# Optimization experiments

Hardware: AMD Instinct MI355X
Metric: run time of the kernel (lower is better)

## Reference

```python
import jax, jax.numpy as jnp
import numpy as np

TEMPERATURE = 0.5
EPS = 1e-8  # F.cosine_similarity default eps
NEG_FILL = -1e9  # fill_diagonal_(-1000000000.0)


def setup_inputs() -> dict:
    key = jax.random.key(0)
    k1, k2 = jax.random.split(key)
    N, D = 4096, 256
    zi = jax.random.normal(k1, (N, D), dtype=jnp.float32)
    zj = jax.random.normal(k2, (N, D), dtype=jnp.float32)
    return {"zi": zi, "zj": zj}


def reference(zi, zj):
    N = zi.shape[0]
    z = jnp.concatenate([zi, zj], axis=0)  # [2N, D]
    # cosine similarity: normalize once, then a single GEMM
    norms = jnp.sqrt(jnp.sum(z * z, axis=1, keepdims=True))
    zn = z / jnp.maximum(norms, EPS)
    sim = jnp.matmul(zn, zn.T) / TEMPERATURE  # [2N, 2N]
    idx = jnp.arange(2 * N)
    sim = sim.at[idx, idx].set(NEG_FILL)  # mask self-similarity
    labels = jnp.concatenate([jnp.arange(N) + N, jnp.arange(N)])
    # CrossEntropyLoss(reduction='sum'): sum_i (logsumexp(row_i) - row_i[label_i])
    logp = jax.nn.log_softmax(sim, axis=1)
    loss = -jnp.sum(logp[idx, labels])
    return loss / (2 * N)
```

## Files before the change

kernel.cpp:

```cpp
#include <hip/hip_runtime.h>
#include <hip/hip_bf16.h>
#include <math.h>


using short8  = __attribute__((ext_vector_type(8))) short;
using floatx4 = __attribute__((ext_vector_type(4))) float;

constexpr int TWO_N = 8192;
constexpr int DIM   = 256;
constexpr int NB    = 64;
constexpr int NTRI  = NB * (NB + 1) / 2;
constexpr float INV2N = 1.0f / 8192.0f;

__device__ static inline unsigned short f2bf(float f) {
  unsigned u = __float_as_uint(f);
  return (unsigned short)((u + 0x7fffu + ((u >> 16) & 1u)) >> 16);
}

__device__ static inline void async_copy16(const __hip_bfloat16* g, __hip_bfloat16* l) {
  __builtin_amdgcn_global_load_lds(
      (const __attribute__((address_space(1))) void*)(const void*)g,
      (__attribute__((address_space(3))) void*)(void*)l, 16, 0, 0);
}

__global__ __launch_bounds__(256) void k_normalize(
    const float* __restrict__ zi, const float* __restrict__ zj,
    __hip_bfloat16* __restrict__ zn, float* __restrict__ rowtotal,
    float* __restrict__ out)
{
  if (blockIdx.x == 0 && threadIdx.x == 0) out[0] = 0.0f;
  if (blockIdx.x < 32) rowtotal[blockIdx.x * 256 + threadIdx.x] = 0.0f;

  const int lane = threadIdx.x & 63;
  const int wave = threadIdx.x >> 6;
  const int row  = blockIdx.x * 4 + wave;
  const float* src = (row < 4096) ? (zi + (size_t)row * DIM)
                                  : (zj + (size_t)(row - 4096) * DIM);
  float4 v = reinterpret_cast<const float4*>(src)[lane];
  float ss = v.x * v.x + v.y * v.y + v.z * v.z + v.w * v.w;
#pragma unroll
  for (int m = 32; m >= 1; m >>= 1) ss += __shfl_xor(ss, m, 64);
  float inv = 1.0f / fmaxf(sqrtf(ss), 1e-8f);
  ushort4 o;
  o.x = f2bf(v.x * inv); o.y = f2bf(v.y * inv);
  o.z = f2bf(v.z * inv); o.w = f2bf(v.w * inv);
  reinterpret_cast<ushort4*>(zn + (size_t)row * DIM)[lane] = o;
}

__global__ __launch_bounds__(256) void k_simexp(
    const __hip_bfloat16* __restrict__ Z, float* __restrict__ rowtotal,
    float* __restrict__ out)
{
  __shared__ __align__(16) __hip_bfloat16 As[128 * 64];
  __shared__ __align__(16) __hip_bfloat16 Bs[128 * 64];
  __shared__ float rowsum[128];
  __shared__ float colsum[128];

  const int tid  = threadIdx.x;
  const int lane = tid & 63;
  const int wave = tid >> 6;
  const int wm   = wave >> 1;
  const int wn   = wave & 1;

  const int u = blockIdx.x;
  int jb = (int)((sqrtf(8.0f * (float)u + 1.0f) - 1.0f) * 0.5f);
  while ((jb + 1) * (jb + 2) / 2 <= u) ++jb;
  while (jb * (jb + 1) / 2 > u) --jb;
  const int ib = u - jb * (jb + 1) / 2;

  const bool diagblk = (ib == jb);
  const bool pairblk = (jb == ib + 32);
  const int i0 = ib * 128;
  const int j0 = jb * 128;

  if (tid < 128) { rowsum[tid] = 0.0f; colsum[tid] = 0.0f; }

  floatx4 acc[4][4] = {};

  const int lane7 = lane & 7;
  const int sub   = lane >> 3;
  const int gkoff = ((lane7 ^ sub) << 3);
  const int q     = lane >> 4;
  const int c16   = lane & 15;

  const __hip_bfloat16* gbase =
      Z + (size_t)((wave < 2 ? i0 : j0) + (wave & 1) * 64) * DIM;
  __hip_bfloat16* lbase = ((wave < 2) ? As : Bs) + (wave & 1) * 64 * 64;

  for (int kk = 0; kk < 4; ++kk) {
    const int k0 = kk * 64;
#pragma unroll
    for (int c = 0; c < 8; ++c) {
      const __hip_bfloat16* gp = gbase + (size_t)(c * 8 + sub) * DIM + k0 + gkoff;
      async_copy16(gp, lbase + c * 512);
    }
    __syncthreads();

#pragma unroll
    for (int ks = 0; ks < 2; ++ks) {
      const int phys = (ks * 4 + q) ^ lane7;
      short8 a[4], b[4];
#pragma unroll
      for (int mt = 0; mt < 4; ++mt)
        a[mt] = *reinterpret_cast<const short8*>(
            As + (wm * 64 + mt * 16 + c16) * 64 + phys * 8);
#pragma unroll
      for (int nt = 0; nt < 4; ++nt)
        b[nt] = *reinterpret_cast<const short8*>(
            Bs + (wn * 64 + nt * 16 + c16) * 64 + phys * 8);
#pragma unroll
      for (int mt = 0; mt < 4; ++mt)
#pragma unroll
        for (int nt = 0; nt < 4; ++nt)
          acc[mt][nt] = __builtin_amdgcn_mfma_f32_16x16x32_bf16(
              a[mt], b[nt], acc[mt][nt], 0, 0, 0);
    }
    __syncthreads();
  }

  float colacc[4] = {0.f, 0.f, 0.f, 0.f};
  float pc = 0.f;
  const bool diagwave = (wm == wn);

#pragma unroll
  for (int mt = 0; mt < 4; ++mt) {
#pragma unroll
    for (int reg = 0; reg < 4; ++reg) {
      const bool onquad = (c16 == q * 4 + reg);
      float s = 0.0f;
#pragma unroll
      for (int nt = 0; nt < 4; ++nt) {
        float e = __expf(2.0f * acc[mt][nt][reg] - 2.0f);
        bool skip = diagblk && diagwave && (nt == mt) && onquad;
        s += skip ? 0.0f : e;
        colacc[nt] += e;
      }
      if (pairblk && diagwave && onquad) pc += acc[mt][mt][reg];
      s += __shfl_xor(s, 1, 64);
      s += __shfl_xor(s, 2, 64);
      s += __shfl_xor(s, 4, 64);
      s += __shfl_xor(s, 8, 64);
      if (c16 == 0)
        atomicAdd(&rowsum[wm * 64 + mt * 16 + q * 4 + reg], s);
    }
  }

  if (!diagblk) {
#pragma unroll
    for (int nt = 0; nt < 4; ++nt) {
      float cs = colacc[nt];
      cs += __shfl_xor(cs, 16, 64);
      cs += __shfl_xor(cs, 32, 64);
      if (lane < 16) atomicAdd(&colsum[wn * 64 + nt * 16 + lane], cs);
    }
  }

  if (pairblk && diagwave) {
#pragma unroll
    for (int m = 32; m >= 1; m >>= 1) pc += __shfl_xor(pc, m, 64);
    if (lane == 0) atomicAdd(out, -4.0f * pc * INV2N);
  }

  __syncthreads();
  if (tid < 128) {
    atomicAdd(&rowtotal[i0 + tid], rowsum[tid]);
    if (!diagblk) atomicAdd(&rowtotal[j0 + tid], colsum[tid]);
  }
}

__global__ __launch_bounds__(256) void k_finalize(
    const float* __restrict__ rowtotal, float* __restrict__ out)
{
  __shared__ float wsum[4];
  const int lane = threadIdx.x & 63;
  const int wave = threadIdx.x >> 6;
  const int row  = blockIdx.x * 256 + threadIdx.x;
  float v = 2.0f + __logf(rowtotal[row]);
#pragma unroll
  for (int m = 32; m >= 1; m >>= 1) v += __shfl_xor(v, m, 64);
  if (lane == 0) wsum[wave] = v;
  __syncthreads();
  if (threadIdx.x == 0)
    atomicAdd(out, (wsum[0] + wsum[1] + wsum[2] + wsum[3]) * INV2N);
}

extern "C" void kernel_launch(void* const* d_in, const int* in_sizes, int n_in,
                              void* d_out, int out_size, void* d_ws, size_t ws_size,
                              hipStream_t stream) {
  const float* zi = (const float*)d_in[0];
  const float* zj = (const float*)d_in[1];
  float* out = (float*)d_out;

  __hip_bfloat16* zn = (__hip_bfloat16*)d_ws;
  float* rowtotal = (float*)((char*)d_ws + (size_t)TWO_N * DIM * 2);

  k_normalize<<<dim3(TWO_N / 4), dim3(256), 0, stream>>>(zi, zj, zn, rowtotal, out);
  k_simexp<<<dim3(NTRI), dim3(256), 0, stream>>>(zn, rowtotal, out);
  k_finalize<<<dim3(TWO_N / 256), dim3(256), 0, stream>>>(rowtotal, out);
}
```

Before: 103.8 us.

## Use 256x128 triangular tiles with per-element diagonal masking in sim-exp kernel

```diff
diff --git a/kernel.cpp b/kernel.cpp
--- a/kernel.cpp
+++ b/kernel.cpp
@@ -8,8 +8,7 @@
 
 constexpr int TWO_N = 8192;
 constexpr int DIM   = 256;
-constexpr int NB    = 64;
-constexpr int NTRI  = NB * (NB + 1) / 2;
+constexpr int NBLKS = 1056;
 constexpr float INV2N = 1.0f / 8192.0f;
 
 __device__ static inline unsigned short f2bf(float f) {
@@ -47,14 +46,14 @@
   reinterpret_cast<ushort4*>(zn + (size_t)row * DIM)[lane] = o;
 }
 
-__global__ __launch_bounds__(256) void k_simexp(
+__global__ __launch_bounds__(256, 2) void k_simexp(
     const __hip_bfloat16* __restrict__ Z, float* __restrict__ rowtotal,
     float* __restrict__ out)
 {
-  __shared__ __align__(16) __hip_bfloat16 As[128 * 64];
+  __shared__ __align__(16) __hip_bfloat16 As[256 * 64];
   __shared__ __align__(16) __hip_bfloat16 Bs[128 * 64];
-  __shared__ float rowsum[128];
-  __shared__ float colsum[128];
+  __shared__ float rowsum[2][256];
+  __shared__ float colsum[2][128];
 
   const int tid  = threadIdx.x;
   const int lane = tid & 63;
@@ -63,19 +62,17 @@
   const int wn   = wave & 1;
 
   const int u = blockIdx.x;
-  int jb = (int)((sqrtf(8.0f * (float)u + 1.0f) - 1.0f) * 0.5f);
-  while ((jb + 1) * (jb + 2) / 2 <= u) ++jb;
-  while (jb * (jb + 1) / 2 > u) --jb;
-  const int ib = u - jb * (jb + 1) / 2;
+  int ib = (int)((65.0f - sqrtf(4225.0f - 4.0f * (float)u)) * 0.5f);
+  while ((ib + 1) * (64 - ib) <= u) ++ib;
+  while (ib * (65 - ib) > u) --ib;
+  const int jb = 2 * ib + (u - ib * (65 - ib));
 
-  const bool diagblk = (ib == jb);
-  const bool pairblk = (jb == ib + 32);
-  const int i0 = ib * 128;
+  const int i0 = ib * 256;
   const int j0 = jb * 128;
+  const bool neardiag = (jb <= 2 * ib + 1);
+  const bool pairblk  = (jb == 2 * ib + 32) || (jb == 2 * ib + 33);
 
-  if (tid < 128) { rowsum[tid] = 0.0f; colsum[tid] = 0.0f; }
-
-  floatx4 acc[4][4] = {};
+  floatx4 acc[8][4] = {};
 
   const int lane7 = lane & 7;
   const int sub   = lane >> 3;
@@ -83,33 +80,33 @@
   const int q     = lane >> 4;
   const int c16   = lane & 15;
 
-  const __hip_bfloat16* gbase =
-      Z + (size_t)((wave < 2 ? i0 : j0) + (wave & 1) * 64) * DIM;
-  __hip_bfloat16* lbase = ((wave < 2) ? As : Bs) + (wave & 1) * 64 * 64;
-
   for (int kk = 0; kk < 4; ++kk) {
     const int k0 = kk * 64;
 #pragma unroll
-    for (int c = 0; c < 8; ++c) {
-      const __hip_bfloat16* gp = gbase + (size_t)(c * 8 + sub) * DIM + k0 + gkoff;
-      async_copy16(gp, lbase + c * 512);
+    for (int c = 0; c < 12; ++c) {
+      const int t = wave * 12 + c;
+      const bool isA = (t < 32);
+      const int seg = isA ? t : (t - 32);
+      const __hip_bfloat16* gp =
+          Z + (size_t)((isA ? i0 : j0) + seg * 8 + sub) * DIM + k0 + gkoff;
+      async_copy16(gp, (isA ? As : Bs) + seg * 512);
     }
     __syncthreads();
 
 #pragma unroll
     for (int ks = 0; ks < 2; ++ks) {
       const int phys = (ks * 4 + q) ^ lane7;
-      short8 a[4], b[4];
+      short8 a[8], b[4];
 #pragma unroll
-      for (int mt = 0; mt < 4; ++mt)
+      for (int mt = 0; mt < 8; ++mt)
         a[mt] = *reinterpret_cast<const short8*>(
-            As + (wm * 64 + mt * 16 + c16) * 64 + phys * 8);
+            As + (wm * 128 + mt * 16 + c16) * 64 + phys * 8);
 #pragma unroll
       for (int nt = 0; nt < 4; ++nt)
         b[nt] = *reinterpret_cast<const short8*>(
             Bs + (wn * 64 + nt * 16 + c16) * 64 + phys * 8);
 #pragma unroll
-      for (int mt = 0; mt < 4; ++mt)
+      for (int mt = 0; mt < 8; ++mt)
 #pragma unroll
         for (int nt = 0; nt < 4; ++nt)
           acc[mt][nt] = __builtin_amdgcn_mfma_f32_16x16x32_bf16(
@@ -120,52 +117,51 @@
 
   float colacc[4] = {0.f, 0.f, 0.f, 0.f};
   float pc = 0.f;
-  const bool diagwave = (wm == wn);
+  const int ibase = i0 + wm * 128 + (q << 2);
+  const int jbase = j0 + wn * 64 + c16;
 
 #pragma unroll
-  for (int mt = 0; mt < 4; ++mt) {
+  for (int mt = 0; mt < 8; ++mt) {
 #pragma unroll
     for (int reg = 0; reg < 4; ++reg) {
-      const bool onquad = (c16 == q * 4 + reg);
+      const int i = ibase + mt * 16 + reg;
       float s = 0.0f;
 #pragma unroll
       for (int nt = 0; nt < 4; ++nt) {
+        const int j = jbase + nt * 16;
         float e = __expf(2.0f * acc[mt][nt][reg] - 2.0f);
-        bool skip = diagblk && diagwave && (nt == mt) && onquad;
-        s += skip ? 0.0f : e;
+        if (neardiag && j <= i) e = 0.0f;
+        s += e;
         colacc[nt] += e;
+        if (pairblk && (j - i == 4096)) pc += acc[mt][nt][reg];
       }
-      if (pairblk && diagwave && onquad) pc += acc[mt][mt][reg];
       s += __shfl_xor(s, 1, 64);
       s += __shfl_xor(s, 2, 64);
       s += __shfl_xor(s, 4, 64);
       s += __shfl_xor(s, 8, 64);
       if (c16 == 0)
-        atomicAdd(&rowsum[wm * 64 + mt * 16 + q * 4 + reg], s);
+        rowsum[wn][wm * 128 + mt * 16 + (q << 2) + reg] = s;
     }
   }
 
-  if (!diagblk) {
 #pragma unroll
-    for (int nt = 0; nt < 4; ++nt) {
-      float cs = colacc[nt];
-      cs += __shfl_xor(cs, 16, 64);
-      cs += __shfl_xor(cs, 32, 64);
-      if (lane < 16) atomicAdd(&colsum[wn * 64 + nt * 16 + lane], cs);
-    }
+  for (int nt = 0; nt < 4; ++nt) {
+    float cs = colacc[nt];
+    cs += __shfl_xor(cs, 16, 64);
+    cs += __shfl_xor(cs, 32, 64);
+    if (lane < 16) colsum[wm][wn * 64 + nt * 16 + lane] = cs;
   }
 
-  if (pairblk && diagwave) {
+  if (pairblk) {
 #pragma unroll
     for (int m = 32; m >= 1; m >>= 1) pc += __shfl_xor(pc, m, 64);
     if (lane == 0) atomicAdd(out, -4.0f * pc * INV2N);
   }
 
   __syncthreads();
-  if (tid < 128) {
-    atomicAdd(&rowtotal[i0 + tid], rowsum[tid]);
-    if (!diagblk) atomicAdd(&rowtotal[j0 + tid], colsum[tid]);
-  }
+  atomicAdd(&rowtotal[i0 + tid], rowsum[0][tid] + rowsum[1][tid]);
+  if (tid < 128)
+    atomicAdd(&rowtotal[j0 + tid], colsum[0][tid] + colsum[1][tid]);
 }
 
 __global__ __launch_bounds__(256) void k_finalize(
@@ -195,6 +191,6 @@
   float* rowtotal = (float*)((char*)d_ws + (size_t)TWO_N * DIM * 2);
 
   k_normalize<<<dim3(TWO_N / 4), dim3(256), 0, stream>>>(zi, zj, zn, rowtotal, out);
-  k_simexp<<<dim3(NTRI), dim3(256), 0, stream>>>(zn, rowtotal, out);
+  k_simexp<<<dim3(NBLKS), dim3(256), 0, stream>>>(zn, rowtotal, out);
   k_finalize<<<dim3(TWO_N / 256), dim3(256), 0, stream>>>(rowtotal, out);
 }
```

Result: slower. 112.1 us (+8.0%).

## Load GEMM fragments directly from global into registers with double buffering, drop LDS staging

Applied to the files above, without the earlier changes.

```diff
diff --git a/kernel.cpp b/kernel.cpp
--- a/kernel.cpp
+++ b/kernel.cpp
@@ -15,12 +15,6 @@
 __device__ static inline unsigned short f2bf(float f) {
   unsigned u = __float_as_uint(f);
   return (unsigned short)((u + 0x7fffu + ((u >> 16) & 1u)) >> 16);
-}
-
-__device__ static inline void async_copy16(const __hip_bfloat16* g, __hip_bfloat16* l) {
-  __builtin_amdgcn_global_load_lds(
-      (const __attribute__((address_space(1))) void*)(const void*)g,
-      (__attribute__((address_space(3))) void*)(void*)l, 16, 0, 0);
 }
 
 __global__ __launch_bounds__(256) void k_normalize(
@@ -51,16 +45,16 @@
     const __hip_bfloat16* __restrict__ Z, float* __restrict__ rowtotal,
     float* __restrict__ out)
 {
-  __shared__ __align__(16) __hip_bfloat16 As[128 * 64];
-  __shared__ __align__(16) __hip_bfloat16 Bs[128 * 64];
-  __shared__ float rowsum[128];
-  __shared__ float colsum[128];
+  __shared__ float rowsum[2][128];
+  __shared__ float colsum[2][128];
 
   const int tid  = threadIdx.x;
   const int lane = tid & 63;
   const int wave = tid >> 6;
   const int wm   = wave >> 1;
   const int wn   = wave & 1;
+  const int c16  = lane & 15;
+  const int q    = lane >> 4;
 
   const int u = blockIdx.x;
   int jb = (int)((sqrtf(8.0f * (float)u + 1.0f) - 1.0f) * 0.5f);
@@ -73,89 +67,77 @@
   const int i0 = ib * 128;
   const int j0 = jb * 128;
 
-  if (tid < 128) { rowsum[tid] = 0.0f; colsum[tid] = 0.0f; }
+  const __hip_bfloat16* pA = Z + (size_t)(i0 + wm * 64 + c16) * DIM + q * 8;
+  const __hip_bfloat16* pB = Z + (size_t)(j0 + wn * 64 + c16) * DIM + q * 8;
 
   floatx4 acc[4][4] = {};
+  short8 a0[4], b0[4], a1[4], b1[4];
 
-  const int lane7 = lane & 7;
-  const int sub   = lane >> 3;
-  const int gkoff = ((lane7 ^ sub) << 3);
-  const int q     = lane >> 4;
-  const int c16   = lane & 15;
+#define LOADF(A_, B_, s_)                                                     \
+  do {                                                                        \
+    _Pragma("unroll") for (int mt = 0; mt < 4; ++mt)                          \
+        A_[mt] = *reinterpret_cast<const short8*>(pA + mt * 16 * DIM + (s_) * 32); \
+    _Pragma("unroll") for (int nt = 0; nt < 4; ++nt)                          \
+        B_[nt] = *reinterpret_cast<const short8*>(pB + nt * 16 * DIM + (s_) * 32); \
+  } while (0)
 
-  const __hip_bfloat16* gbase =
-      Z + (size_t)((wave < 2 ? i0 : j0) + (wave & 1) * 64) * DIM;
-  __hip_bfloat16* lbase = ((wave < 2) ? As : Bs) + (wave & 1) * 64 * 64;
+#define MFMAF(A_, B_)                                                         \
+  do {                                                                        \
+    _Pragma("unroll") for (int mt = 0; mt < 4; ++mt)                          \
+        _Pragma("unroll") for (int nt = 0; nt < 4; ++nt)                      \
+            acc[mt][nt] = __builtin_amdgcn_mfma_f32_16x16x32_bf16(            \
+                A_[mt], B_[nt], acc[mt][nt], 0, 0, 0);                        \
+  } while (0)
 
-  for (int kk = 0; kk < 4; ++kk) {
-    const int k0 = kk * 64;
+  LOADF(a0, b0, 0);
 #pragma unroll
-    for (int c = 0; c < 8; ++c) {
-      const __hip_bfloat16* gp = gbase + (size_t)(c * 8 + sub) * DIM + k0 + gkoff;
-      async_copy16(gp, lbase + c * 512);
-    }
-    __syncthreads();
-
-#pragma unroll
-    for (int ks = 0; ks < 2; ++ks) {
-      const int phys = (ks * 4 + q) ^ lane7;
-      short8 a[4], b[4];
-#pragma unroll
-      for (int mt = 0; mt < 4; ++mt)
-        a[mt] = *reinterpret_cast<const short8*>(
-            As + (wm * 64 + mt * 16 + c16) * 64 + phys * 8);
-#pragma unroll
-      for (int nt = 0; nt < 4; ++nt)
-        b[nt] = *reinterpret_cast<const short8*>(
-            Bs + (wn * 64 + nt * 16 + c16) * 64 + phys * 8);
-#pragma unroll
-      for (int mt = 0; mt < 4; ++mt)
-#pragma unroll
-        for (int nt = 0; nt < 4; ++nt)
-          acc[mt][nt] = __builtin_amdgcn_mfma_f32_16x16x32_bf16(
-              a[mt], b[nt], acc[mt][nt], 0, 0, 0);
-    }
-    __syncthreads();
+  for (int s = 0; s < 8; s += 2) {
+    if (s + 1 < 8) LOADF(a1, b1, s + 1);
+    MFMAF(a0, b0);
+    if (s + 2 < 8) LOADF(a0, b0, s + 2);
+    MFMAF(a1, b1);
   }
+#undef LOADF
+#undef MFMAF
 
   float colacc[4] = {0.f, 0.f, 0.f, 0.f};
   float pc = 0.f;
-  const bool diagwave = (wm == wn);
+  const int ibase = i0 + wm * 64 + (q << 2);
+  const int jbase = j0 + wn * 64 + c16;
 
 #pragma unroll
   for (int mt = 0; mt < 4; ++mt) {
 #pragma unroll
     for (int reg = 0; reg < 4; ++reg) {
-      const bool onquad = (c16 == q * 4 + reg);
+      const int i = ibase + mt * 16 + reg;
       float s = 0.0f;
 #pragma unroll
       for (int nt = 0; nt < 4; ++nt) {
+        const int j = jbase + nt * 16;
         float e = __expf(2.0f * acc[mt][nt][reg] - 2.0f);
-        bool skip = diagblk && diagwave && (nt == mt) && onquad;
-        s += skip ? 0.0f : e;
+        if (diagblk && j <= i) e = 0.0f;
+        s += e;
         colacc[nt] += e;
+        if (pairblk && (j - i == 4096)) pc += acc[mt][nt][reg];
       }
-      if (pairblk && diagwave && onquad) pc += acc[mt][mt][reg];
       s += __shfl_xor(s, 1, 64);
       s += __shfl_xor(s, 2, 64);
       s += __shfl_xor(s, 4, 64);
       s += __shfl_xor(s, 8, 64);
       if (c16 == 0)
-        atomicAdd(&rowsum[wm * 64 + mt * 16 + q * 4 + reg], s);
+        rowsum[wn][wm * 64 + mt * 16 + (q << 2) + reg] = s;
     }
   }
 
-  if (!diagblk) {
 #pragma unroll
-    for (int nt = 0; nt < 4; ++nt) {
-      float cs = colacc[nt];
-      cs += __shfl_xor(cs, 16, 64);
-      cs += __shfl_xor(cs, 32, 64);
-      if (lane < 16) atomicAdd(&colsum[wn * 64 + nt * 16 + lane], cs);
-    }
+  for (int nt = 0; nt < 4; ++nt) {
+    float cs = colacc[nt];
+    cs += __shfl_xor(cs, 16, 64);
+    cs += __shfl_xor(cs, 32, 64);
+    if (lane < 16) colsum[wm][wn * 64 + nt * 16 + lane] = cs;
   }
 
-  if (pairblk && diagwave) {
+  if (pairblk) {
 #pragma unroll
     for (int m = 32; m >= 1; m >>= 1) pc += __shfl_xor(pc, m, 64);
     if (lane == 0) atomicAdd(out, -4.0f * pc * INV2N);
@@ -163,8 +145,8 @@
 
   __syncthreads();
   if (tid < 128) {
-    atomicAdd(&rowtotal[i0 + tid], rowsum[tid]);
-    if (!diagblk) atomicAdd(&rowtotal[j0 + tid], colsum[tid]);
+    atomicAdd(&rowtotal[i0 + tid], rowsum[0][tid] + rowsum[1][tid]);
+    atomicAdd(&rowtotal[j0 + tid], colsum[0][tid] + colsum[1][tid]);
   }
 }
 
```

After: 141.8 us. 1.37x slower.

## Fuse normalize, sim-exp and finalize into one persistent kernel with grid barriers

Applied to the files above, without the earlier changes.

```diff
diff --git a/kernel.cpp b/kernel.cpp
--- a/kernel.cpp
+++ b/kernel.cpp
@@ -8,8 +8,8 @@
 
 constexpr int TWO_N = 8192;
 constexpr int DIM   = 256;
-constexpr int NB    = 64;
-constexpr int NTRI  = NB * (NB + 1) / 2;
+constexpr int GRID  = 520;
+constexpr int TPB   = 4;
 constexpr float INV2N = 1.0f / 8192.0f;
 
 __device__ static inline unsigned short f2bf(float f) {
@@ -23,33 +23,22 @@
       (__attribute__((address_space(3))) void*)(void*)l, 16, 0, 0);
 }
 
-__global__ __launch_bounds__(256) void k_normalize(
+__device__ static inline void gridbar(unsigned* bar, unsigned target) {
+  __syncthreads();
+  if (threadIdx.x == 0) {
+    __threadfence();
+    __hip_atomic_fetch_add(bar, 1u, __ATOMIC_ACQ_REL, __HIP_MEMORY_SCOPE_AGENT);
+    while (__hip_atomic_load(bar, __ATOMIC_ACQUIRE, __HIP_MEMORY_SCOPE_AGENT) < target)
+      __builtin_amdgcn_s_sleep(8);
+    __threadfence();
+  }
+  __syncthreads();
+}
+
+__global__ __launch_bounds__(256, 3) void k_fused(
     const float* __restrict__ zi, const float* __restrict__ zj,
     __hip_bfloat16* __restrict__ zn, float* __restrict__ rowtotal,
-    float* __restrict__ out)
-{
-  if (blockIdx.x == 0 && threadIdx.x == 0) out[0] = 0.0f;
-  if (blockIdx.x < 32) rowtotal[blockIdx.x * 256 + threadIdx.x] = 0.0f;
-
-  const int lane = threadIdx.x & 63;
-  const int wave = threadIdx.x >> 6;
-  const int row  = blockIdx.x * 4 + wave;
-  const float* src = (row < 4096) ? (zi + (size_t)row * DIM)
-                                  : (zj + (size_t)(row - 4096) * DIM);
-  float4 v = reinterpret_cast<const float4*>(src)[lane];
-  float ss = v.x * v.x + v.y * v.y + v.z * v.z + v.w * v.w;
-#pragma unroll
-  for (int m = 32; m >= 1; m >>= 1) ss += __shfl_xor(ss, m, 64);
-  float inv = 1.0f / fmaxf(sqrtf(ss), 1e-8f);
-  ushort4 o;
-  o.x = f2bf(v.x * inv); o.y = f2bf(v.y * inv);
-  o.z = f2bf(v.z * inv); o.w = f2bf(v.w * inv);
-  reinterpret_cast<ushort4*>(zn + (size_t)row * DIM)[lane] = o;
-}
-
-__global__ __launch_bounds__(256) void k_simexp(
-    const __hip_bfloat16* __restrict__ Z, float* __restrict__ rowtotal,
-    float* __restrict__ out)
+    unsigned* __restrict__ bar, float* __restrict__ out)
 {
   __shared__ __align__(16) __hip_bfloat16 As[128 * 64];
   __shared__ __align__(16) __hip_bfloat16 Bs[128 * 64];
@@ -59,129 +48,150 @@
   const int tid  = threadIdx.x;
   const int lane = tid & 63;
   const int wave = tid >> 6;
-  const int wm   = wave >> 1;
-  const int wn   = wave & 1;
-
-  const int u = blockIdx.x;
-  int jb = (int)((sqrtf(8.0f * (float)u + 1.0f) - 1.0f) * 0.5f);
-  while ((jb + 1) * (jb + 2) / 2 <= u) ++jb;
-  while (jb * (jb + 1) / 2 > u) --jb;
-  const int ib = u - jb * (jb + 1) / 2;
-
-  const bool diagblk = (ib == jb);
-  const bool pairblk = (jb == ib + 32);
-  const int i0 = ib * 128;
-  const int j0 = jb * 128;
-
-  if (tid < 128) { rowsum[tid] = 0.0f; colsum[tid] = 0.0f; }
-
-  floatx4 acc[4][4] = {};
-
+
+#pragma unroll
+  for (int it = 0; it < 4; ++it) {
+    const int row = blockIdx.x * 16 + it * 4 + wave;
+    if (row < TWO_N) {
+      const float* src = (row < 4096) ? (zi + (size_t)row * DIM)
+                                      : (zj + (size_t)(row - 4096) * DIM);
+      float4 v = reinterpret_cast<const float4*>(src)[lane];
+      float ss = v.x * v.x + v.y * v.y + v.z * v.z + v.w * v.w;
+#pragma unroll
+      for (int m = 32; m >= 1; m >>= 1) ss += __shfl_xor(ss, m, 64);
+      float inv = 1.0f / fmaxf(sqrtf(ss), 1e-8f);
+      ushort4 o;
+      o.x = f2bf(v.x * inv); o.y = f2bf(v.y * inv);
+      o.z = f2bf(v.z * inv); o.w = f2bf(v.w * inv);
+      reinterpret_cast<ushort4*>(zn + (size_t)row * DIM)[lane] = o;
+    }
+  }
+  if (blockIdx.x < 32) rowtotal[blockIdx.x * 256 + tid] = 0.0f;
+  if (blockIdx.x == 0 && tid == 0) out[0] = 0.0f;
+
+  gridbar(bar, GRID);
+
+  const int wm  = wave >> 1;
+  const int wn  = wave & 1;
+  const int c16 = lane & 15;
+  const int q   = lane >> 4;
   const int lane7 = lane & 7;
   const int sub   = lane >> 3;
   const int gkoff = ((lane7 ^ sub) << 3);
-  const int q     = lane >> 4;
-  const int c16   = lane & 15;
-
-  const __hip_bfloat16* gbase =
-      Z + (size_t)((wave < 2 ? i0 : j0) + (wave & 1) * 64) * DIM;
-  __hip_bfloat16* lbase = ((wave < 2) ? As : Bs) + (wave & 1) * 64 * 64;
-
-  for (int kk = 0; kk < 4; ++kk) {
-    const int k0 = kk * 64;
-#pragma unroll
-    for (int c = 0; c < 8; ++c) {
-      const __hip_bfloat16* gp = gbase + (size_t)(c * 8 + sub) * DIM + k0 + gkoff;
-      async_copy16(gp, lbase + c * 512);
-    }
+
+  for (int t = 0; t < TPB; ++t) {
+    const int u = blockIdx.x * TPB + t;
+    int jb = (int)((sqrtf(8.0f * (float)u + 1.0f) - 1.0f) * 0.5f);
+    while ((jb + 1) * (jb + 2) / 2 <= u) ++jb;
+    while (jb * (jb + 1) / 2 > u) --jb;
+    const int ib = u - jb * (jb + 1) / 2;
+
+    const bool diagblk = (ib == jb);
+    const bool pairblk = (jb == ib + 32);
+    const int i0 = ib * 128;
+    const int j0 = jb * 128;
+
+    if (tid < 128) { rowsum[tid] = 0.0f; colsum[tid] = 0.0f; }
+
+    floatx4 acc[4][4] = {};
+
+    const __hip_bfloat16* gbase =
+        zn + (size_t)((wave < 2 ? i0 : j0) + (wave & 1) * 64) * DIM;
+    __hip_bfloat16* lbase = ((wave < 2) ? As : Bs) + (wave & 1) * 64 * 64;
+
+    for (int kk = 0; kk < 4; ++kk) {
+      const int k0 = kk * 64;
+#pragma unroll
+      for (int c = 0; c < 8; ++c) {
+        const __hip_bfloat16* gp = gbase + (size_t)(c * 8 + sub) * DIM + k0 + gkoff;
+        async_copy16(gp, lbase + c * 512);
+      }
+      __syncthreads();
+
+#pragma unroll
+      for (int ks = 0; ks < 2; ++ks) {
+        const int phys = (ks * 4 + q) ^ lane7;
+        short8 a[4], b[4];
+#pragma unroll
+        for (int mt = 0; mt < 4; ++mt)
+          a[mt] = *reinterpret_cast<const short8*>(
+              As + (wm * 64 + mt * 16 + c16) * 64 + phys * 8);
+#pragma unroll
+        for (int nt = 0; nt < 4; ++nt)
+          b[nt] = *reinterpret_cast<const short8*>(
+              Bs + (wn * 64 + nt * 16 + c16) * 64 + phys * 8);
+#pragma unroll
+        for (int mt = 0; mt < 4; ++mt)
+#pragma unroll
+          for (int nt = 0; nt < 4; ++nt)
+            acc[mt][nt] = __builtin_amdgcn_mfma_f32_16x16x32_bf16(
+                a[mt], b[nt], acc[mt][nt], 0, 0, 0);
+      }
+      __syncthreads();
+    }
+
+    float colacc[4] = {0.f, 0.f, 0.f, 0.f};
+    float pc = 0.f;
+    const bool diagwave = (wm == wn);
+
+#pragma unroll
+    for (int mt = 0; mt < 4; ++mt) {
+#pragma unroll
+      for (int reg = 0; reg < 4; ++reg) {
+        const bool onquad = (c16 == q * 4 + reg);
+        float s = 0.0f;
+#pragma unroll
+        for (int nt = 0; nt < 4; ++nt) {
+          float e = __expf(2.0f * acc[mt][nt][reg] - 2.0f);
+          bool skip = diagblk && diagwave && (nt == mt) && onquad;
+          s += skip ? 0.0f : e;
+          colacc[nt] += e;
+        }
+        if (pairblk && diagwave && onquad) pc += acc[mt][mt][reg];
+        s += __shfl_xor(s, 1, 64);
+        s += __shfl_xor(s, 2, 64);
+        s += __shfl_xor(s, 4, 64);
+        s += __shfl_xor(s, 8, 64);
+        if (c16 == 0)
+          atomicAdd(&rowsum[wm * 64 + mt * 16 + q * 4 + reg], s);
+      }
+    }
+
+    if (!diagblk) {
+#pragma unroll
+      for (int nt = 0; nt < 4; ++nt) {
+        float cs = colacc[nt];
+        cs += __shfl_xor(cs, 16, 64);
+        cs += __shfl_xor(cs, 32, 64);
+        if (lane < 16) atomicAdd(&colsum[wn * 64 + nt * 16 + lane], cs);
+      }
+    }
+
+    if (pairblk && diagwave) {
+#pragma unroll
+      for (int m = 32; m >= 1; m >>= 1) pc += __shfl_xor(pc, m, 64);
+      if (lane == 0) atomicAdd(out, -4.0f * pc * INV2N);
+    }
+
     __syncthreads();
-
-#pragma unroll
-    for (int ks = 0; ks < 2; ++ks) {
-      const int phys = (ks * 4 + q) ^ lane7;
-      short8 a[4], b[4];
-#pragma unroll
-      for (int mt = 0; mt < 4; ++mt)
-        a[mt] = *reinterpret_cast<const short8*>(
-            As + (wm * 64 + mt * 16 + c16) * 64 + phys * 8);
-#pragma unroll
-      for (int nt = 0; nt < 4; ++nt)
-        b[nt] = *reinterpret_cast<const short8*>(
-            Bs + (wn * 64 + nt * 16 + c16) * 64 + phys * 8);
-#pragma unroll
-      for (int mt = 0; mt < 4; ++mt)
-#pragma unroll
-        for (int nt = 0; nt < 4; ++nt)
-          acc[mt][nt] = __builtin_amdgcn_mfma_f32_16x16x32_bf16(
-              a[mt], b[nt], acc[mt][nt], 0, 0, 0);
-    }
-    __syncthreads();
-  }
-
-  float colacc[4] = {0.f, 0.f, 0.f, 0.f};
-  float pc = 0.f;
-  const bool diagwave = (wm == wn);
-
-#pragma unroll
-  for (int mt = 0; mt < 4; ++mt) {
-#pragma unroll
-    for (int reg = 0; reg < 4; ++reg) {
-      const bool onquad = (c16 == q * 4 + reg);
-      float s = 0.0f;
-#pragma unroll
-      for (int nt = 0; nt < 4; ++nt) {
-        float e = __expf(2.0f * acc[mt][nt][reg] - 2.0f);
-        bool skip = diagblk && diagwave && (nt == mt) && onquad;
-        s += skip ? 0.0f : e;
-        colacc[nt] += e;
-      }
-      if (pairblk && diagwave && onquad) pc += acc[mt][mt][reg];
-      s += __shfl_xor(s, 1, 64);
-      s += __shfl_xor(s, 2, 64);
-      s += __shfl_xor(s, 4, 64);
-      s += __shfl_xor(s, 8, 64);
-      if (c16 == 0)
-        atomicAdd(&rowsum[wm * 64 + mt * 16 + q * 4 + reg], s);
-    }
-  }
-
-  if (!diagblk) {
-#pragma unroll
-    for (int nt = 0; nt < 4; ++nt) {
-      float cs = colacc[nt];
-      cs += __shfl_xor(cs, 16, 64);
-      cs += __shfl_xor(cs, 32, 64);
-      if (lane < 16) atomicAdd(&colsum[wn * 64 + nt * 16 + lane], cs);
-    }
-  }
-
-  if (pairblk && diagwave) {
-#pragma unroll
-    for (int m = 32; m >= 1; m >>= 1) pc += __shfl_xor(pc, m, 64);
-    if (lane == 0) atomicAdd(out, -4.0f * pc * INV2N);
-  }
-
-  __syncthreads();
-  if (tid < 128) {
-    atomicAdd(&rowtotal[i0 + tid], rowsum[tid]);
-    if (!diagblk) atomicAdd(&rowtotal[j0 + tid], colsum[tid]);
-  }
-}
-
-__global__ __launch_bounds__(256) void k_finalize(
-    const float* __restrict__ rowtotal, float* __restrict__ out)
-{
-  __shared__ float wsum[4];
-  const int lane = threadIdx.x & 63;
-  const int wave = threadIdx.x >> 6;
-  const int row  = blockIdx.x * 256 + threadIdx.x;
-  float v = 2.0f + __logf(rowtotal[row]);
-#pragma unroll
-  for (int m = 32; m >= 1; m >>= 1) v += __shfl_xor(v, m, 64);
-  if (lane == 0) wsum[wave] = v;
-  __syncthreads();
-  if (threadIdx.x == 0)
-    atomicAdd(out, (wsum[0] + wsum[1] + wsum[2] + wsum[3]) * INV2N);
+    if (tid < 128) {
+      atomicAdd(&rowtotal[i0 + tid], rowsum[tid]);
+      if (!diagblk) atomicAdd(&rowtotal[j0 + tid], colsum[tid]);
+    }
+  }
+
+  gridbar(bar, 2 * GRID);
+
+  if (wave == 0) {
+    const int row = blockIdx.x * 16 + tid;
+    float v = 0.0f;
+    if (tid < 16 && row < TWO_N) v = 2.0f + __logf(rowtotal[row]);
+    v += __shfl_xor(v, 1, 64);
+    v += __shfl_xor(v, 2, 64);
+    v += __shfl_xor(v, 4, 64);
+    v += __shfl_xor(v, 8, 64);
+    if (lane == 0) atomicAdd(out, v * INV2N);
+  }
 }
 
 extern "C" void kernel_launch(void* const* d_in, const int* in_sizes, int n_in,
@@ -193,8 +203,8 @@
 
   __hip_bfloat16* zn = (__hip_bfloat16*)d_ws;
   float* rowtotal = (float*)((char*)d_ws + (size_t)TWO_N * DIM * 2);
-
-  k_normalize<<<dim3(TWO_N / 4), dim3(256), 0, stream>>>(zi, zj, zn, rowtotal, out);
-  k_simexp<<<dim3(NTRI), dim3(256), 0, stream>>>(zn, rowtotal, out);
-  k_finalize<<<dim3(TWO_N / 256), dim3(256), 0, stream>>>(rowtotal, out);
-}
+  unsigned* bar = (unsigned*)((char*)d_ws + (size_t)TWO_N * DIM * 2 + TWO_N * 4);
+
+  hipMemsetAsync(bar, 0, sizeof(unsigned), stream);
+  k_fused<<<dim3(GRID), dim3(256), 0, stream>>>(zi, zj, zn, rowtotal, bar, out);
+}
```

After: 221.3 us. 113% more time.
